# Kernel tuning notes

Hardware: AMD Instinct MI355X
Metric: run time of the kernel (lower is better)

## Reference

```python
import jax, jax.numpy as jnp
import numpy as np

B, N_PER, F_IN, HID, DEG = 64, 1024, 64, 128, 16
N = B * N_PER
E = N * DEG

def _ceil_k(k):
    return -((-4 * k) // 5)  # ceil(0.8 * k), static python int

def setup_inputs():
    key = jax.random.key(0)
    ks = jax.random.split(key, 16)
    x = jax.random.normal(ks[0], (N, F_IN), jnp.float32)
    # edges are intra-graph: local endpoints in [0, N_PER) offset by graph id
    loc = jax.random.randint(ks[1], (2, E), 0, N_PER, jnp.int32)
    gid = jnp.repeat(jnp.arange(B, dtype=jnp.int32), E // B)
    edge_index = loc + gid[None, :] * N_PER
    batch = jnp.repeat(jnp.arange(B, dtype=jnp.int32), N_PER)
    def lin(k, fi, fo):
        s = 1.0 / float(np.sqrt(fi))
        return jax.random.uniform(k, (fi, fo), jnp.float32, -s, s)
    inp = dict(x=x, edge_index=edge_index, batch=batch)
    inp["Wr1"] = lin(ks[2], F_IN, HID); inp["Wn1"] = lin(ks[3], F_IN, HID); inp["b1"] = jnp.zeros((HID,), jnp.float32)
    inp["Wr2"] = lin(ks[4], HID, HID); inp["Wn2"] = lin(ks[5], HID, HID); inp["b2"] = jnp.zeros((HID,), jnp.float32)
    inp["Wr3"] = lin(ks[6], HID, HID); inp["Wn3"] = lin(ks[7], HID, HID); inp["b3"] = jnp.zeros((HID,), jnp.float32)
    inp["p1"] = jax.random.normal(ks[8], (HID,), jnp.float32)
    inp["p2"] = jax.random.normal(ks[9], (HID,), jnp.float32)
    inp["p3"] = jax.random.normal(ks[10], (HID,), jnp.float32)
    inp["l1w"] = lin(ks[11], 2 * HID, HID); inp["l1b"] = jnp.zeros((HID,), jnp.float32)
    inp["l2w"] = lin(ks[12], HID, 2); inp["l2b"] = jnp.zeros((2,), jnp.float32)
    return inp

def _graph_conv(x, src, dst, emask, Wr, Wn, b, n_nodes):
    # x'_i = W1 x_i + sum_{j->i} W2 x_j + b ; masked edges contribute 0
    msg = x[src] * emask[:, None]                                  # [E, H]
    agg = jax.ops.segment_sum(msg, dst, num_segments=n_nodes)     # [N, H]
    return x @ Wr + agg @ Wn + b

def _topk_pool(x, src, dst, emask, p, k_prev):
    # PyG TopKPooling: score = x.p/||p||, keep ceil(0.8*n) per graph,
    # x_out = x[perm] * tanh(score[perm]); relabel+filter edges
    k_new = _ceil_k(k_prev)
    s = (x @ p) / jnp.linalg.norm(p)                               # [B*k_prev]
    vals, idx = jax.lax.top_k(s.reshape(B, k_prev), k_new)        # [B, k_new]
    perm = (idx + jnp.arange(B, dtype=idx.dtype)[:, None] * k_prev).reshape(-1)
    x_new = x[perm] * jnp.tanh(vals.reshape(-1))[:, None]
    inv = jnp.full((B * k_prev,), -1, jnp.int32).at[perm].set(jnp.arange(B * k_new, dtype=jnp.int32))
    ns, nd = inv[src], inv[dst]
    valid = emask * ((ns >= 0) & (nd >= 0)).astype(x.dtype)
    return x_new, jnp.maximum(ns, 0), jnp.maximum(nd, 0), valid, k_new

def _readout(x, k):
    b = jnp.repeat(jnp.arange(B, dtype=jnp.int32), k)
    gmax = jax.ops.segment_max(x, b, num_segments=B)
    gmean = jax.ops.segment_sum(x, b, num_segments=B) / k
    return jnp.concatenate([gmax, gmean], axis=1)                  # [B, 2H]

def reference(x, edge_index, batch, Wr1, Wn1, b1, Wr2, Wn2, b2, Wr3, Wn3, b3, p1, p2, p3, l1w, l1b, l2w, l2b):
    src, dst = edge_index[0], edge_index[1]
    emask = jnp.ones((E,), x.dtype)
    k = N_PER
    convs = [(Wr1, Wn1, b1), (Wr2, Wn2, b2), (Wr3, Wn3, b3)]
    pools = [p1, p2, p3]
    xs = []
    for (Wr, Wn, bb), p in zip(convs, pools):
        x = jax.nn.relu(_graph_conv(x, src, dst, emask, Wr, Wn, bb, B * k))
        x, src, dst, emask, k = _topk_pool(x, src, dst, emask, p, k)
        xs.append(_readout(x, k))
    h = xs[0] + xs[1] + xs[2]
    h = jax.nn.relu(h @ l1w + l1b)
    # F.dropout(p=0.5) skipped: eval-mode reference
    h = jax.nn.relu(h @ l2w + l2b)
    return jax.nn.log_softmax(h, axis=-1)
```

## Files before the change

kernel.cpp:

```cpp
#include <hip/hip_runtime.h>
#include <hip/hip_bf16.h>
#include <math.h>

#define NN   65536
#define NPER 1024
#define NE   1048576
#define NB   64
#define EPG  16384

typedef __attribute__((ext_vector_type(8))) short short8;
typedef __attribute__((ext_vector_type(4))) float f32x4;


__global__ __launch_bounds__(1024) void csr_kernel(const int* __restrict__ ei,
      int* __restrict__ off, int* __restrict__ adj){
  __shared__ int hist[1024];
  __shared__ int wsum[16];
  const int g = ((int)blockIdx.x & 7)*8 + ((int)blockIdx.x >> 3);
  const int t = threadIdx.x;
  const int ebase = g*EPG, nbase = g*NPER;
  hist[t] = 0;
  __syncthreads();
  int srcs[16], dls[16];
  #pragma unroll
  for (int i = 0; i < 16; ++i){
    int e = ebase + t + i*1024;
    srcs[i] = ei[e];
    dls[i]  = ei[NE + e] - nbase;
    atomicAdd(&hist[dls[i]], 1);
  }
  __syncthreads();
  int v = hist[t];
  int lane = t & 63, wid = t >> 6;
  int s = v;
  #pragma unroll
  for (int d = 1; d < 64; d <<= 1){
    int src = (lane >= d) ? (lane - d) : lane;
    int u = __shfl(s, src);
    if (lane >= d) s += u;
  }
  if (lane == 63) wsum[wid] = s;
  __syncthreads();
  if (wid == 0){
    int ws = (lane < 16) ? wsum[lane] : 0;
    #pragma unroll
    for (int d = 1; d < 16; d <<= 1){
      int src = (lane >= d) ? (lane - d) : lane;
      int u = __shfl(ws, src);
      if (lane >= d) ws += u;
    }
    if (lane < 16) wsum[lane] = ws;
  }
  __syncthreads();
  int base = (wid > 0) ? wsum[wid - 1] : 0;
  int excl = base + s - v;
  __syncthreads();
  hist[t] = excl;
  off[nbase + t] = ebase + excl;
  if (g == NB - 1 && t == 1023) off[NN] = NE;
  __syncthreads();
  #pragma unroll
  for (int i = 0; i < 16; ++i){
    int pos = atomicAdd(&hist[dls[i]], 1);
    adj[ebase + pos] = srcs[i];
  }
}


__global__ __launch_bounds__(1024) void gather_kernel(const float* __restrict__ x, int F,
      const int* __restrict__ off, const int* __restrict__ adjB, const float* __restrict__ scl,
      const int* __restrict__ deg2, float* __restrict__ agg, const int* __restrict__ alive){
  int bid = blockIdx.x;
  bid = (bid & 7) * (gridDim.x >> 3) + (bid >> 3);
  int w = bid*16 + ((int)threadIdx.x >> 6);
  int lane = threadIdx.x & 63;
  if (alive && !alive[w]) return;
  int s0 = off[w];
  int s1 = deg2 ? (s0 + deg2[w]) : off[w+1];
  if (F == 64){
    const char* xb = (const char*)x + (lane & 15)*16;
    int sub = lane >> 4;
    float4 a0 = make_float4(0.f,0.f,0.f,0.f), a1 = a0;
    if (s1 > s0){
      for (int e = s0; e < s1; e += 8){
        int e0 = e + sub, e1 = e + 4 + sub;
        bool ok0 = e0 < s1, ok1 = e1 < s1;
        size_t oA = (size_t)(unsigned)adjB[ok0 ? e0 : (s1 - 1)] << 8;
        size_t oB = (size_t)(unsigned)adjB[ok1 ? e1 : (s1 - 1)] << 8;
        float t0 = ok0 ? 1.f : 0.f, t1 = ok1 ? 1.f : 0.f;
        float4 vA = *(const float4*)(xb + oA);
        float4 vB = *(const float4*)(xb + oB);
        a0.x = fmaf(vA.x, t0, a0.x); a0.y = fmaf(vA.y, t0, a0.y);
        a0.z = fmaf(vA.z, t0, a0.z); a0.w = fmaf(vA.w, t0, a0.w);
        a1.x = fmaf(vB.x, t1, a1.x); a1.y = fmaf(vB.y, t1, a1.y);
        a1.z = fmaf(vB.z, t1, a1.z); a1.w = fmaf(vB.w, t1, a1.w);
      }
    }
    a0.x += a1.x; a0.y += a1.y; a0.z += a1.z; a0.w += a1.w;
    #pragma unroll
    for (int m = 16; m <= 32; m <<= 1){
      a0.x += __shfl_xor(a0.x, m);
      a0.y += __shfl_xor(a0.y, m);
      a0.z += __shfl_xor(a0.z, m);
      a0.w += __shfl_xor(a0.w, m);
    }
    if (lane < 16) *(float4*)&agg[(size_t)w*128 + (lane & 15)*4] = a0;
  } else {
    const char* xb = (const char*)x + (lane & 31)*16;
    int sub = lane >> 5;
    float4 a[4];
    #pragma unroll
    for (int i = 0; i < 4; ++i) a[i] = make_float4(0.f,0.f,0.f,0.f);
    if (s1 > s0){
      for (int e = s0; e < s1; e += 8){
        int ss[4]; float tv[4];
        #pragma unroll
        for (int i = 0; i < 4; ++i){
          int ei = e + 2*i + sub;
          bool okE = ei < s1;
          int ii = okE ? ei : (s1 - 1);
          ss[i] = adjB[ii];
          tv[i] = okE ? scl[ii] : 0.f;
        }
        #pragma unroll
        for (int i = 0; i < 4; ++i){
          float4 v = *(const float4*)(xb + (size_t)(unsigned)ss[i]);
          a[i].x = fmaf(v.x, tv[i], a[i].x);
          a[i].y = fmaf(v.y, tv[i], a[i].y);
          a[i].z = fmaf(v.z, tv[i], a[i].z);
          a[i].w = fmaf(v.w, tv[i], a[i].w);
        }
      }
    }
    float4 r;
    r.x = (a[0].x + a[1].x) + (a[2].x + a[3].x);
    r.y = (a[0].y + a[1].y) + (a[2].y + a[3].y);
    r.z = (a[0].z + a[1].z) + (a[2].z + a[3].z);
    r.w = (a[0].w + a[1].w) + (a[2].w + a[3].w);
    r.x += __shfl_xor(r.x, 32);
    r.y += __shfl_xor(r.y, 32);
    r.z += __shfl_xor(r.z, 32);
    r.w += __shfl_xor(r.w, 32);
    if (lane < 32) *(float4*)&agg[(size_t)w*128 + (lane & 31)*4] = r;
  }
}


__global__ __launch_bounds__(256) void wsplit_all_kernel(
      const float* __restrict__ Wr0, const float* __restrict__ Wn0,
      const float* __restrict__ Wr1, const float* __restrict__ Wn1,
      const float* __restrict__ Wr2, const float* __restrict__ Wn2,
      unsigned short* __restrict__ WTh, unsigned short* __restrict__ WTl){
  int idx = blockIdx.x*256 + threadIdx.x;
  int rel, Kcat, Kx, base;
  const float *Wr, *Wn;
  if (idx < 16384){ rel = idx;          Kcat = 128; Kx = 64;  base = 0;     Wr = Wr0; Wn = Wn0; }
  else if (idx < 49152){ rel = idx - 16384; Kcat = 256; Kx = 128; base = 16384; Wr = Wr1; Wn = Wn1; }
  else { rel = idx - 49152; Kcat = 256; Kx = 128; base = 49152; Wr = Wr2; Wn = Wn2; }
  int c = rel & 127, k = rel >> 7;
  float w = (k < Kx) ? Wr[k*128 + c] : Wn[(k - Kx)*128 + c];
  __hip_bfloat16 h = __float2bfloat16(w);
  float hf = __bfloat162float(h);
  __hip_bfloat16 l = __float2bfloat16(w - hf);
  WTh[base + c*Kcat + k] = reinterpret_cast<unsigned short&>(h);
  WTl[base + c*Kcat + k] = reinterpret_cast<unsigned short&>(l);
}


__global__ __launch_bounds__(256, 2) void conv_kernel(const float* __restrict__ xsrc, int strideX, int ntx,
      const float* aggb, int nta,
      const unsigned short* __restrict__ WTh, const unsigned short* __restrict__ WTl, int Kcat,
      const float* __restrict__ bias, const float* __restrict__ p, const float* __restrict__ scaleX,
      float* yout, float* __restrict__ score){
  __shared__ unsigned short XhL[128*32], XlL[128*32];
  __shared__ unsigned short WhL[128*32], WlL[128*32];
  __shared__ float sbuf[128*2];
  const int tid = threadIdx.x;
  const int rblk = ((int)blockIdx.x & 7) * ((int)gridDim.x >> 3) + ((int)blockIdx.x >> 3);
  const int row0 = rblk * 128;
  const int srow = tid & 127;
  const int shalf = tid >> 7;
  const int lane = tid & 63;
  const int wid = tid >> 6;
  const int wr = wid >> 1, wc = wid & 1;
  const int l15 = lane & 15, lkq = lane >> 4;

  const float xscale = scaleX ? scaleX[row0 + srow] : 1.f;

  f32x4 acc[4][4];
  #pragma unroll
  for (int m = 0; m < 4; ++m)
    #pragma unroll
    for (int j = 0; j < 4; ++j)
      acc[m][j] = (f32x4){0.f, 0.f, 0.f, 0.f};

  const int nt = ntx + nta;
  for (int t = 0; t < nt; ++t){
    __syncthreads();
    {
      const float* Xs   = (t < ntx) ? xsrc : aggb;
      const int stride  = (t < ntx) ? strideX : 128;
      const int kc      = (t < ntx) ? t*32 : (t - ntx)*32;
      const float sc    = (t < ntx) ? xscale : 1.f;
      #pragma unroll
      for (int kq2 = 0; kq2 < 2; ++kq2){
        const int kq = shalf*2 + kq2;
        const float* xp = Xs + (size_t)(row0 + srow)*stride + kc + kq*8;
        float4 v0 = *(const float4*)(xp);
        float4 v1 = *(const float4*)(xp + 4);
        float vv[8] = {v0.x*sc, v0.y*sc, v0.z*sc, v0.w*sc,
                       v1.x*sc, v1.y*sc, v1.z*sc, v1.w*sc};
        short8 hs, ls;
        #pragma unroll
        for (int q = 0; q < 8; ++q){
          __hip_bfloat16 h = __float2bfloat16(vv[q]);
          float hf = __bfloat162float(h);
          __hip_bfloat16 lo = __float2bfloat16(vv[q] - hf);
          hs[q] = reinterpret_cast<short&>(h);
          ls[q] = reinterpret_cast<short&>(lo);
        }
        const int kqph = kq ^ (srow & 3);
        *(short8*)&XhL[srow*32 + kqph*8] = hs;
        *(short8*)&XlL[srow*32 + kqph*8] = ls;
      }
      const int kcw = t*32;
      #pragma unroll
      for (int kq2 = 0; kq2 < 2; ++kq2){
        const int kq = shalf*2 + kq2;
        short8 h = *(const short8*)&WTh[(size_t)srow*Kcat + kcw + kq*8];
        short8 l = *(const short8*)&WTl[(size_t)srow*Kcat + kcw + kq*8];
        const int kqph = kq ^ (srow & 3);
        *(short8*)&WhL[srow*32 + kqph*8] = h;
        *(short8*)&WlL[srow*32 + kqph*8] = l;
      }
    }
    __syncthreads();
    short8 bh[4], bl[4];
    #pragma unroll
    for (int j = 0; j < 4; ++j){
      const int col = wc*64 + j*16 + l15;
      const int offb = col*32 + (lkq ^ (col & 3))*8;
      bh[j] = *(const short8*)&WhL[offb];
      bl[j] = *(const short8*)&WlL[offb];
    }
    #pragma unroll
    for (int m = 0; m < 4; ++m){
      const int row = wr*64 + m*16 + l15;
      const int offa = row*32 + (lkq ^ (row & 3))*8;
      short8 ah = *(const short8*)&XhL[offa];
      short8 al = *(const short8*)&XlL[offa];
      #pragma unroll
      for (int j = 0; j < 4; ++j){
        acc[m][j] = __builtin_amdgcn_mfma_f32_16x16x32_bf16(ah, bh[j], acc[m][j], 0, 0, 0);
        acc[m][j] = __builtin_amdgcn_mfma_f32_16x16x32_bf16(ah, bl[j], acc[m][j], 0, 0, 0);
        acc[m][j] = __builtin_amdgcn_mfma_f32_16x16x32_bf16(al, bh[j], acc[m][j], 0, 0, 0);
      }
    }
  }

  #pragma unroll
  for (int m = 0; m < 4; ++m){
    float prt[4] = {0.f, 0.f, 0.f, 0.f};
    #pragma unroll
    for (int j = 0; j < 4; ++j){
      const int col = wc*64 + j*16 + l15;
      const float bcol = bias[col];
      const float pcol = p[col];
      f32x4 a = acc[m][j];
      #pragma unroll
      for (int r = 0; r < 4; ++r){
        const int row = wr*64 + m*16 + lkq*4 + r;
        float y = fmaxf(a[r] + bcol, 0.f);
        yout[(size_t)(row0 + row)*128 + col] = y;
        prt[r] = fmaf(y, pcol, prt[r]);
      }
    }
    #pragma unroll
    for (int r = 0; r < 4; ++r){
      #pragma unroll
      for (int msk = 8; msk >= 1; msk >>= 1) prt[r] += __shfl_xor(prt[r], msk);
      if (l15 == 0) sbuf[(wr*64 + m*16 + lkq*4 + r)*2 + wc] = prt[r];
    }
  }
  __syncthreads();
  if (tid < 128) score[row0 + tid] = sbuf[tid*2] + sbuf[tid*2 + 1];
}


__global__ __launch_bounds__(1024) void tail_kernel(const float* __restrict__ score,
      const int* __restrict__ alive_cur, int* __restrict__ alive_next,
      float* __restrict__ scale, const float* __restrict__ p, int m,
      const float* __restrict__ y, float* __restrict__ h, int firstLevel,
      const int* __restrict__ off, const int* __restrict__ adj,
      int* __restrict__ adj2, float* __restrict__ scl2, int* __restrict__ deg2, int doCompact){
  __shared__ float lv[1024];
  __shared__ int   li[1024];
  __shared__ float sscale[1024];
  __shared__ int   salive[1024];
  __shared__ float smx[8*128];
  __shared__ float ssm[8*128];
  __shared__ float rnorm;
  const int g = ((int)blockIdx.x & 7)*8 + ((int)blockIdx.x >> 3);
  const int t = threadIdx.x;
  if (t < 64){
    float v0 = p[t], v1 = p[t + 64];
    float ss = v0*v0 + v1*v1;
    #pragma unroll
    for (int mm = 32; mm >= 1; mm >>= 1) ss += __shfl_xor(ss, mm);
    if (t == 0) rnorm = rsqrtf(ss);
  }
  sscale[t] = 0.f;
  salive[t] = 0;
  const int node = g*NPER + t;
  bool ok = alive_cur ? (alive_cur[node] != 0) : true;
  float v = ok ? score[node] : -INFINITY;
  int idx = node;
  alive_next[node] = 0;
  scale[node] = 0.f;
  __syncthreads();

  auto cex_shfl = [&](int stride, bool dirUp){
    float vj = __shfl_xor(v, stride);
    int   ij = __shfl_xor(idx, stride);
    bool iAmLow = (t & stride) == 0;
    bool mineFirst = (v > vj) || (v == vj && idx < ij);
    bool takeMine = ((dirUp == iAmLow) == mineFirst);
    v   = takeMine ? v   : vj;
    idx = takeMine ? idx : ij;
  };
  auto cex_lds = [&](int stride, bool dirUp){
    __syncthreads();
    lv[t] = v; li[t] = idx;
    __syncthreads();
    float vj = lv[t ^ stride];
    int   ij = li[t ^ stride];
    bool iAmLow = (t & stride) == 0;
    bool mineFirst = (v > vj) || (v == vj && idx < ij);
    bool takeMine = ((dirUp == iAmLow) == mineFirst);
    v   = takeMine ? v   : vj;
    idx = takeMine ? idx : ij;
  };

  #pragma unroll
  for (int size = 2; size <= 64; size <<= 1){
    const bool dirUp = (t & size) == 0;
    for (int stride = size >> 1; stride >= 1; stride >>= 1)
      cex_shfl(stride, dirUp);
  }
  #pragma unroll
  for (int size = 128; size <= 1024; size <<= 1){
    const bool dirUp = (t & size) == 0;
    for (int stride = size >> 1; stride >= 64; stride >>= 1)
      cex_lds(stride, dirUp);
    for (int stride = 32; stride >= 1; stride >>= 1)
      cex_shfl(stride, dirUp);
  }

  if (t < m){
    float tv = tanhf(v * rnorm);
    alive_next[idx] = 1;
    scale[idx] = tv;
    int loc = idx - g*NPER;
    sscale[loc] = tv;
    salive[loc] = 1;
  }
  __syncthreads();

  {
    const int f = t & 127, grp = t >> 7;
    const int nb0 = grp*128;
    const float* yg = y + (size_t)(g*NPER)*128 + f;
    float mx[4] = {-INFINITY, -INFINITY, -INFINITY, -INFINITY};
    float sm[4] = {0.f, 0.f, 0.f, 0.f};
    #pragma unroll 4
    for (int i = 0; i < 128; i += 4){
      #pragma unroll
      for (int q = 0; q < 4; ++q){
        int nl = nb0 + i + q;
        float o = yg[(size_t)nl*128] * sscale[nl];
        mx[q] = salive[nl] ? fmaxf(mx[q], o) : mx[q];
        sm[q] += o;
      }
    }
    float mxa = fmaxf(fmaxf(mx[0], mx[1]), fmaxf(mx[2], mx[3]));
    float sma = (sm[0] + sm[1]) + (sm[2] + sm[3]);
    smx[grp*128 + f] = mxa; ssm[grp*128 + f] = sma;
    __syncthreads();
    #pragma unroll
    for (int s2 = 4; s2 >= 1; s2 >>= 1){
      if (grp < s2){
        smx[grp*128 + f] = fmaxf(smx[grp*128 + f], smx[(grp+s2)*128 + f]);
        ssm[grp*128 + f] += ssm[(grp+s2)*128 + f];
      }
      __syncthreads();
    }
    if (grp == 0){
      if (firstLevel){
        h[g*256 + f]       = smx[f];
        h[g*256 + 128 + f] = ssm[f] / (float)m;
      } else {
        h[g*256 + f]       += smx[f];
        h[g*256 + 128 + f] += ssm[f] / (float)m;
      }
    }
  }

  if (doCompact){
    const int lane2 = t & 63, wv = t >> 6;
    for (int n2 = 0; n2 < 64; ++n2){
      int wl = wv*64 + n2;
      int w = g*NPER + wl;
      if (!salive[wl]){ if (lane2 == 0) deg2[w] = 0; continue; }
      int s0 = off[w], s1 = off[w+1];
      int bse = s0;
      for (int e0 = s0; e0 < s1; e0 += 64){
        int e = e0 + lane2;
        bool okE = e < s1;
        int sN = adj[okE ? e : (s1 - 1)];
        float tv = sscale[sN - g*NPER];
        bool keep = okE && (tv != 0.f);
        unsigned long long mmask = __ballot(keep);
        int pos = bse + __popcll(mmask & ((1ull << lane2) - 1ull));
        if (keep){ adj2[pos] = sN << 9; scl2[pos] = tv; }
        bse += __popcll(mmask);
      }
      if (lane2 == 0) deg2[w] = bse - s0;
    }
  }
}


__global__ __launch_bounds__(128) void final_kernel(const float* __restrict__ h,
      const float* __restrict__ l1w, const float* __restrict__ l1b,
      const float* __restrict__ l2w, const float* __restrict__ l2b,
      float* __restrict__ out){
  int g = blockIdx.x, t = threadIdx.x;
  __shared__ float hrow[256];
  __shared__ float red0[128], red1[128];
  hrow[t]       = h[g*256 + t];
  hrow[t + 128] = h[g*256 + 128 + t];
  __syncthreads();
  float a = l1b[t];
  for (int k = 0; k < 256; ++k) a = fmaf(hrow[k], l1w[k*128 + t], a);
  a = fmaxf(a, 0.f);
  red0[t] = a * l2w[t*2 + 0];
  red1[t] = a * l2w[t*2 + 1];
  __syncthreads();
  for (int s = 64; s > 0; s >>= 1){
    if (t < s){ red0[t] += red0[t + s]; red1[t] += red1[t + s]; }
    __syncthreads();
  }
  if (t == 0){
    float z0 = fmaxf(red0[0] + l2b[0], 0.f);
    float z1 = fmaxf(red1[0] + l2b[1], 0.f);
    float mz = fmaxf(z0, z1);
    float lse = mz + logf(expf(z0 - mz) + expf(z1 - mz));
    out[g*2 + 0] = z0 - lse;
    out[g*2 + 1] = z1 - lse;
  }
}


static inline size_t alignup(size_t x){ return (x + 255) & ~(size_t)255; }

extern "C" void kernel_launch(void* const* d_in, const int* in_sizes, int n_in,
                              void* d_out, int out_size, void* d_ws, size_t ws_size,
                              hipStream_t stream) {
  const float* x_in = (const float*)d_in[0];
  const int*   ei   = (const int*)d_in[1];
  const float* Wr[3] = {(const float*)d_in[3], (const float*)d_in[6], (const float*)d_in[9]};
  const float* Wn[3] = {(const float*)d_in[4], (const float*)d_in[7], (const float*)d_in[10]};
  const float* bs[3] = {(const float*)d_in[5], (const float*)d_in[8], (const float*)d_in[11]};
  const float* ps[3] = {(const float*)d_in[12], (const float*)d_in[13], (const float*)d_in[14]};
  const float* l1w = (const float*)d_in[15];
  const float* l1b = (const float*)d_in[16];
  const float* l2w = (const float*)d_in[17];
  const float* l2b = (const float*)d_in[18];
  float* out = (float*)d_out;

  char* w = (char*)d_ws;
  size_t o = 0;
  auto take = [&](size_t bytes) -> void* { void* p = w + o; o = alignup(o + bytes); return p; };
  int*   off    = (int*)  take((size_t)(NN + 1) * 4);
  int*   adj    = (int*)  take((size_t)NE * 4);
  int*   adj2   = (int*)  take((size_t)NE * 4);
  float* scl2   = (float*)take((size_t)NE * 4);
  int*   deg2   = (int*)  take((size_t)NN * 4);
  int*   aliveA = (int*)  take((size_t)NN * 4);
  int*   aliveB = (int*)  take((size_t)NN * 4);
  float* scale  = (float*)take((size_t)NN * 4);
  float* score  = (float*)take((size_t)NN * 4);
  float* h      = (float*)take((size_t)NB * 256 * 4);
  unsigned short* WTh = (unsigned short*)take((size_t)81920 * 2);
  unsigned short* WTl = (unsigned short*)take((size_t)81920 * 2);
  float* A      = (float*)take((size_t)NN * 128 * 4);
  float* Bb     = (float*)take((size_t)NN * 128 * 4);
  (void)ws_size; (void)n_in; (void)in_sizes; (void)out_size;

  csr_kernel<<<NB, 1024, 0, stream>>>(ei, off, adj);
  wsplit_all_kernel<<<320, 256, 0, stream>>>(Wr[0], Wn[0], Wr[1], Wn[1], Wr[2], Wn[2], WTh, WTl);

  const int MS[3]   = {820, 656, 525};
  const int WOFF[3] = {0, 16384, 49152};
  const int KCAT[3] = {128, 256, 256};
  int* aliveCur = nullptr;
  int* aliveNext = aliveA;
  float* bufs[2] = {Bb, A};
  for (int l = 0; l < 3; ++l){
    const int Kx = (l == 0) ? 64 : 128;
    const int Ka = (l == 0) ? 64 : 128;
    float* aggb = bufs[l & 1];
    if (l == 0){
      gather_kernel<<<NN/16, 1024, 0, stream>>>(x_in, 64, off, adj, nullptr, nullptr, aggb, nullptr);
      conv_kernel<<<NN/128, 256, 0, stream>>>(x_in, 64, Kx/32, aggb, Ka/32, WTh + WOFF[0], WTl + WOFF[0], KCAT[0],
                                              bs[0], ps[0], nullptr, aggb, score);
    } else {
      const float* ysrc = bufs[(l - 1) & 1];
      gather_kernel<<<NN/16, 1024, 0, stream>>>(ysrc, 128, off, adj2, scl2, deg2, aggb, aliveCur);
      conv_kernel<<<NN/128, 256, 0, stream>>>(ysrc, 128, Kx/32, aggb, Ka/32, WTh + WOFF[l], WTl + WOFF[l], KCAT[l],
                                              bs[l], ps[l], scale, aggb, score);
    }
    tail_kernel<<<NB, 1024, 0, stream>>>(score, aliveCur, aliveNext, scale, ps[l], MS[l],
                                         aggb, h, (l == 0) ? 1 : 0,
                                         off, adj, adj2, scl2, deg2, (l < 2) ? 1 : 0);
    aliveCur = aliveNext;
    aliveNext = (l == 0) ? aliveB : aliveA;
  }
  final_kernel<<<NB, 128, 0, stream>>>(h, l1w, l1b, l2w, l2b, out);
}
```

Baseline: 319.0 us.

## Split per-graph tail kernel into topk, readout and compaction kernels

The old tail kernel ran top-k selection, pooled readout and edge compaction in one kernel with only 64 blocks, one per graph. This splits it into three kernels. Readout now runs on 64x8 blocks over a selected-index list, so it reads only the kept rows, and compaction runs on 4096 blocks with one wave per node. This raises parallelism for the memory-heavy readout and compaction phases, at the cost of two extra launches per level and an extra global selList buffer.

```diff
diff --git a/kernel.cpp b/kernel.cpp
--- a/kernel.cpp
+++ b/kernel.cpp
@@ -287,18 +287,12 @@
 }
 
 
-__global__ __launch_bounds__(1024) void tail_kernel(const float* __restrict__ score,
+__global__ __launch_bounds__(1024) void topk_kernel(const float* __restrict__ score,
       const int* __restrict__ alive_cur, int* __restrict__ alive_next,
-      float* __restrict__ scale, const float* __restrict__ p, int m,
-      const float* __restrict__ y, float* __restrict__ h, int firstLevel,
-      const int* __restrict__ off, const int* __restrict__ adj,
-      int* __restrict__ adj2, float* __restrict__ scl2, int* __restrict__ deg2, int doCompact){
+      float* __restrict__ scale, int* __restrict__ selList,
+      const float* __restrict__ p, int m){
   __shared__ float lv[1024];
   __shared__ int   li[1024];
-  __shared__ float sscale[1024];
-  __shared__ int   salive[1024];
-  __shared__ float smx[8*128];
-  __shared__ float ssm[8*128];
   __shared__ float rnorm;
   const int g = ((int)blockIdx.x & 7)*8 + ((int)blockIdx.x >> 3);
   const int t = threadIdx.x;
@@ -309,15 +303,12 @@
     for (int mm = 32; mm >= 1; mm >>= 1) ss += __shfl_xor(ss, mm);
     if (t == 0) rnorm = rsqrtf(ss);
   }
-  sscale[t] = 0.f;
-  salive[t] = 0;
   const int node = g*NPER + t;
   bool ok = alive_cur ? (alive_cur[node] != 0) : true;
   float v = ok ? score[node] : -INFINITY;
   int idx = node;
   alive_next[node] = 0;
   scale[node] = 0.f;
-  __syncthreads();
 
   auto cex_shfl = [&](int stride, bool dirUp){
     float vj = __shfl_xor(v, stride);
@@ -357,76 +348,73 @@
   }
 
   if (t < m){
-    float tv = tanhf(v * rnorm);
     alive_next[idx] = 1;
-    scale[idx] = tv;
-    int loc = idx - g*NPER;
-    sscale[loc] = tv;
-    salive[loc] = 1;
-  }
-  __syncthreads();
-
-  {
-    const int f = t & 127, grp = t >> 7;
-    const int nb0 = grp*128;
-    const float* yg = y + (size_t)(g*NPER)*128 + f;
-    float mx[4] = {-INFINITY, -INFINITY, -INFINITY, -INFINITY};
-    float sm[4] = {0.f, 0.f, 0.f, 0.f};
-    #pragma unroll 4
-    for (int i = 0; i < 128; i += 4){
-      #pragma unroll
-      for (int q = 0; q < 4; ++q){
-        int nl = nb0 + i + q;
-        float o = yg[(size_t)nl*128] * sscale[nl];
-        mx[q] = salive[nl] ? fmaxf(mx[q], o) : mx[q];
-        sm[q] += o;
-      }
-    }
-    float mxa = fmaxf(fmaxf(mx[0], mx[1]), fmaxf(mx[2], mx[3]));
-    float sma = (sm[0] + sm[1]) + (sm[2] + sm[3]);
-    smx[grp*128 + f] = mxa; ssm[grp*128 + f] = sma;
+    scale[idx] = tanhf(v * rnorm);
+    selList[g*NPER + t] = idx;
+  }
+}
+
+
+__global__ __launch_bounds__(1024) void readout_kernel(const float* __restrict__ y,
+      const float* __restrict__ scale, const int* __restrict__ selList,
+      float* __restrict__ h, int m, int firstLevel){
+  __shared__ float smx[64][17];
+  __shared__ float ssm[64][17];
+  int g = ((int)blockIdx.x & 7)*8 + ((int)blockIdx.x >> 3);
+  int fq = blockIdx.y;
+  int t = threadIdx.x;
+  int c  = t >> 4;
+  int lf = t & 15;
+  int f  = fq*16 + lf;
+  const int* sel = selList + g*NPER;
+  float mx = -INFINITY, sm = 0.f;
+  for (int r = c; r < m; r += 64){
+    int node = sel[r];
+    float o = y[(size_t)node*128 + f] * scale[node];
+    mx = fmaxf(mx, o);
+    sm += o;
+  }
+  smx[c][lf] = mx; ssm[c][lf] = sm;
+  __syncthreads();
+  for (int s = 32; s > 0; s >>= 1){
+    if (c < s){
+      smx[c][lf] = fmaxf(smx[c][lf], smx[c+s][lf]);
+      ssm[c][lf] += ssm[c+s][lf];
+    }
     __syncthreads();
-    #pragma unroll
-    for (int s2 = 4; s2 >= 1; s2 >>= 1){
-      if (grp < s2){
-        smx[grp*128 + f] = fmaxf(smx[grp*128 + f], smx[(grp+s2)*128 + f]);
-        ssm[grp*128 + f] += ssm[(grp+s2)*128 + f];
-      }
-      __syncthreads();
-    }
-    if (grp == 0){
-      if (firstLevel){
-        h[g*256 + f]       = smx[f];
-        h[g*256 + 128 + f] = ssm[f] / (float)m;
-      } else {
-        h[g*256 + f]       += smx[f];
-        h[g*256 + 128 + f] += ssm[f] / (float)m;
-      }
-    }
-  }
-
-  if (doCompact){
-    const int lane2 = t & 63, wv = t >> 6;
-    for (int n2 = 0; n2 < 64; ++n2){
-      int wl = wv*64 + n2;
-      int w = g*NPER + wl;
-      if (!salive[wl]){ if (lane2 == 0) deg2[w] = 0; continue; }
-      int s0 = off[w], s1 = off[w+1];
-      int bse = s0;
-      for (int e0 = s0; e0 < s1; e0 += 64){
-        int e = e0 + lane2;
-        bool okE = e < s1;
-        int sN = adj[okE ? e : (s1 - 1)];
-        float tv = sscale[sN - g*NPER];
-        bool keep = okE && (tv != 0.f);
-        unsigned long long mmask = __ballot(keep);
-        int pos = bse + __popcll(mmask & ((1ull << lane2) - 1ull));
-        if (keep){ adj2[pos] = sN << 9; scl2[pos] = tv; }
-        bse += __popcll(mmask);
-      }
-      if (lane2 == 0) deg2[w] = bse - s0;
-    }
-  }
+  }
+  if (c == 0){
+    if (firstLevel){
+      h[g*256 + f]       = smx[0][lf];
+      h[g*256 + 128 + f] = ssm[0][lf] / (float)m;
+    } else {
+      h[g*256 + f]       += smx[0][lf];
+      h[g*256 + 128 + f] += ssm[0][lf] / (float)m;
+    }
+  }
+}
+
+
+__global__ __launch_bounds__(1024) void compact_kernel(const int* __restrict__ off, const int* __restrict__ adj,
+      const float* __restrict__ scale, const int* __restrict__ alive,
+      int* __restrict__ adj2, float* __restrict__ scl2, int* __restrict__ deg2){
+  int w = blockIdx.x*16 + ((int)threadIdx.x >> 6);
+  int lane = threadIdx.x & 63;
+  if (!alive[w]){ if (lane == 0) deg2[w] = 0; return; }
+  int s0 = off[w], s1 = off[w+1];
+  int base = s0;
+  for (int e0 = s0; e0 < s1; e0 += 64){
+    int e = e0 + lane;
+    bool okE = e < s1;
+    int s = adj[okE ? e : (s1 - 1)];
+    float t = scale[s];
+    bool keep = okE && (t != 0.f);
+    unsigned long long m = __ballot(keep);
+    int pos = base + __popcll(m & ((1ull << lane) - 1ull));
+    if (keep){ adj2[pos] = s << 9; scl2[pos] = t; }
+    base += __popcll(m);
+  }
+  if (lane == 0) deg2[w] = base - s0;
 }
 
 
@@ -490,6 +478,7 @@
   int*   aliveB = (int*)  take((size_t)NN * 4);
   float* scale  = (float*)take((size_t)NN * 4);
   float* score  = (float*)take((size_t)NN * 4);
+  int*   selList= (int*)  take((size_t)NN * 4);
   float* h      = (float*)take((size_t)NB * 256 * 4);
   unsigned short* WTh = (unsigned short*)take((size_t)81920 * 2);
   unsigned short* WTl = (unsigned short*)take((size_t)81920 * 2);
@@ -520,9 +509,10 @@
       conv_kernel<<<NN/128, 256, 0, stream>>>(ysrc, 128, Kx/32, aggb, Ka/32, WTh + WOFF[l], WTl + WOFF[l], KCAT[l],
                                               bs[l], ps[l], scale, aggb, score);
     }
-    tail_kernel<<<NB, 1024, 0, stream>>>(score, aliveCur, aliveNext, scale, ps[l], MS[l],
-                                         aggb, h, (l == 0) ? 1 : 0,
-                                         off, adj, adj2, scl2, deg2, (l < 2) ? 1 : 0);
+    topk_kernel<<<NB, 1024, 0, stream>>>(score, aliveCur, aliveNext, scale, selList, ps[l], MS[l]);
+    readout_kernel<<<dim3(NB, 8), 1024, 0, stream>>>(aggb, scale, selList, h, MS[l], (l == 0) ? 1 : 0);
+    if (l < 2)
+      compact_kernel<<<NN/16, 1024, 0, stream>>>(off, adj, scale, aliveNext, adj2, scl2, deg2);
     aliveCur = aliveNext;
     aliveNext = (l == 0) ? aliveB : aliveA;
   }
```

Result: faster. 269.8 us, median of 2 (-15.4%).
